# Performance work log

Measured on AMD Instinct MI355X. Metric: run time of the kernel, lower is better.

Reference implementation:

```python
import jax, jax.numpy as jnp
import numpy as np

N_NODES = 20000
N_EDGES = 160000
IN_DIM = 2048
HID = 512


def setup_inputs() -> dict:
    key = jax.random.key(0)
    ks = jax.random.split(key, 12)
    s1 = 1.0 / np.sqrt(IN_DIM)
    s2 = 1.0 / np.sqrt(HID)
    return {
        "x": jax.random.normal(ks[0], (N_NODES, IN_DIM), dtype=jnp.float32),
        "edge_index": jax.random.randint(ks[1], (2, N_EDGES), 0, N_NODES, dtype=jnp.int64),
        "W1": jax.random.uniform(ks[2], (IN_DIM, HID), jnp.float32, -s1, s1),
        "b1": jax.random.uniform(ks[3], (HID,), jnp.float32, -s1, s1),
        "W2": jax.random.uniform(ks[4], (HID, HID), jnp.float32, -s2, s2),
        "b2": jax.random.uniform(ks[5], (HID,), jnp.float32, -s2, s2),
        "Wg": jax.random.uniform(ks[6], (HID, HID), jnp.float32, -s2, s2),
        "bg": jax.random.uniform(ks[7], (HID,), jnp.float32, -s2, s2),
        "Wa": jax.random.uniform(ks[8], (HID, 1), jnp.float32, -s2, s2),
        "ba": jax.random.uniform(ks[9], (1,), jnp.float32, -s2, s2),
    }


def reference(x, edge_index, W1, b1, W2, b2, Wg, bg, Wa, ba):
    # GINConv (eps=0): h = MLP((1+eps)*x + sum_{j in N(i)} x_j)
    src, dst = edge_index[0], edge_index[1]
    agg = jax.ops.segment_sum(x[src], dst, num_segments=x.shape[0])  # [N, IN_DIM]
    h = x + agg
    h = jnp.maximum(h @ W1 + b1, 0.0) @ W2 + b2  # [N, HID]
    # Gated attention pooling scores
    A = jnp.tanh(h @ Wg + bg)                    # [N, HID]
    alpha = (A @ Wa + ba)[:, 0]                  # [N]
    att_scores = jax.nn.softmax(alpha, axis=0)   # softmax over all nodes
    return (h, att_scores)
```

## Files before the change

### kernel.cpp

```cpp
#include <hip/hip_runtime.h>

typedef __attribute__((ext_vector_type(8))) __bf16 bf16x8;
typedef __attribute__((ext_vector_type(4))) __bf16 bf16x4;
typedef __attribute__((ext_vector_type(4))) float f32x4;
typedef __attribute__((ext_vector_type(8))) unsigned short u16x8;

__device__ __forceinline__ bf16x8 cvt8(float4 a, float4 b) {
    bf16x8 o;
    o[0] = (__bf16)a.x; o[1] = (__bf16)a.y; o[2] = (__bf16)a.z; o[3] = (__bf16)a.w;
    o[4] = (__bf16)b.x; o[5] = (__bf16)b.y; o[6] = (__bf16)b.z; o[7] = (__bf16)b.w;
    return o;
}
__device__ __forceinline__ bf16x4 cvt4(f32x4 v) {
    bf16x4 o;
    o[0] = (__bf16)v[0]; o[1] = (__bf16)v[1]; o[2] = (__bf16)v[2]; o[3] = (__bf16)v[3];
    return o;
}

__device__ __forceinline__ unsigned swz(int row, int s) {
    return (unsigned)((row * 64 + s * 16) ^ ((row & 8) << 2));
}

__global__ __launch_bounds__(256) void convw_pre_kernel(const float* __restrict__ W,
                                                        char* __restrict__ out, int K) {
    int t = blockIdx.x * 256 + threadIdx.x;
    if (t >= K * 512) return;
    int k = t >> 9, n = t & 511;
    int cb = n >> 8, r = n & 255, tt = k >> 5, s = (k & 31) >> 3, e = k & 7;
    size_t off = ((size_t)cb * (K >> 5) + tt) * 16384 + swz(r, s) + e * 2;
    *(__bf16*)(out + off) = (__bf16)W[t];
}

__global__ __launch_bounds__(256) void count_kernel(const int* __restrict__ dst,
                                                    int* __restrict__ counts, int E) {
    int e = blockIdx.x * 256 + threadIdx.x;
    if (e < E) atomicAdd(&counts[dst[e]], 1);
}

__global__ __launch_bounds__(1024) void scan_kernel(const int* __restrict__ counts,
                                                    int* __restrict__ offs, int N) {
    __shared__ int wsum[16], wpre[16];
    const int CH = 20;
    int tid = threadIdx.x, lane = tid & 63, wv = tid >> 6;
    int base = tid * CH;
    int s = 0;
    for (int i = 0; i < CH; i++) { int idx = base + i; s += (idx < N) ? counts[idx] : 0; }
    int run = s;
#pragma unroll
    for (int o = 1; o < 64; o <<= 1) { int v = __shfl_up(run, o, 64); if (lane >= o) run += v; }
    if (lane == 63) wsum[wv] = run;
    __syncthreads();
    if (tid == 0) { int acc = 0; for (int w = 0; w < 16; w++) { wpre[w] = acc; acc += wsum[w]; } }
    __syncthreads();
    int pre = wpre[wv] + (run - s);
    for (int i = 0; i < CH; i++) {
        int idx = base + i;
        if (idx <= N) offs[idx] = pre;
        pre += (idx < N) ? counts[idx] : 0;
    }
}

__global__ __launch_bounds__(256) void bucket_kernel(const int* __restrict__ src,
                                                     const int* __restrict__ dst,
                                                     const int* __restrict__ offs,
                                                     int* __restrict__ cursor,
                                                     int* __restrict__ eids, int E) {
    int e = blockIdx.x * 256 + threadIdx.x;
    if (e >= E) return;
    int d = dst[e];
    int pos = atomicAdd(&cursor[d], 1);
    eids[offs[d] + pos] = src[e];
}

__global__ __launch_bounds__(256) void gather_h1_kernel(const float* __restrict__ y,
                                                        const int* __restrict__ offs,
                                                        const int* __restrict__ eids,
                                                        const float* __restrict__ b1,
                                                        __bf16* __restrict__ h1b,
                                                        int N) {
    int node = blockIdx.x * 2 + (threadIdx.x >> 7);
    if (node >= N) return;
    int c = (threadIdx.x & 127) << 2;
    float4 s = *(const float4*)(y + (size_t)node * 512 + c);
    int beg = offs[node], end = offs[node + 1];
    for (int k = beg; k < end; k++) {
        int sn = eids[k];
        const float4 v = *(const float4*)(y + (size_t)sn * 512 + c);
        s.x += v.x; s.y += v.y; s.z += v.z; s.w += v.w;
    }
    const float4 b = *(const float4*)(b1 + c);
    f32x4 r;
    r[0] = fmaxf(s.x + b.x, 0.f);
    r[1] = fmaxf(s.y + b.y, 0.f);
    r[2] = fmaxf(s.z + b.z, 0.f);
    r[3] = fmaxf(s.w + b.w, 0.f);
    *(bf16x4*)(h1b + (size_t)node * 512 + c) = cvt4(r);
}

template <int KDIM, int AMODE, int EPI>
__global__ __launch_bounds__(256) void gemm_nb(const void* __restrict__ Asrc,
                                               const char* __restrict__ Bpre,
                                               const float* __restrict__ bias,
                                               float* __restrict__ Cf,
                                               const float* __restrict__ Wa,
                                               float* __restrict__ alphaOut,
                                               int M) {
    constexpr int NT2 = KDIM / 64;
    __shared__ char smem[16384];
    const int tid = threadIdx.x, lane = tid & 63, wv = tid >> 6;
    const int fr = lane & 15, sec = lane >> 4, hi4 = (lane >> 4) * 4;
    const long row0 = (long)blockIdx.x * 64;
    const int cb = blockIdx.y;
    const char* Bp = Bpre + (size_t)cb * (KDIM / 32) * 16384;

    f32x4 acc[4][4];
#pragma unroll
    for (int m = 0; m < 4; m++)
#pragma unroll
        for (int n = 0; n < 4; n++)
#pragma unroll
            for (int r = 0; r < 4; r++) acc[m][n][r] = 0.f;

    const int ar_ = tid >> 2, ks = tid & 3;
    const unsigned awz = swz(ar_, ks);
    long arow = row0 + ar_; if (arow > (long)M - 1) arow = M - 1;
    const float* ApF = (const float*)Asrc + arow * KDIM;
    const char*  ApH = (const char*)Asrc + arow * (KDIM * 2);

#define ASEC(b) (smem + (b) * 8192)

    if constexpr (AMODE == 0) {
        float4 a0 = *(const float4*)(ApF + ks * 8);
        float4 a1 = *(const float4*)(ApF + ks * 8 + 4);
        float4 a2 = *(const float4*)(ApF + 32 + ks * 8);
        float4 a3 = *(const float4*)(ApF + 32 + ks * 8 + 4);
        *(bf16x8*)(ASEC(0) + awz) = cvt8(a0, a1);
        *(bf16x8*)(ASEC(0) + 4096 + awz) = cvt8(a2, a3);
    } else {
        u16x8 v0 = *(const u16x8*)(ApH + ks * 16);
        u16x8 v1 = *(const u16x8*)(ApH + 64 + ks * 16);
        *(u16x8*)(ASEC(0) + awz) = v0;
        *(u16x8*)(ASEC(0) + 4096 + awz) = v1;
    }
    asm volatile("s_waitcnt lgkmcnt(0)" ::: "memory");
    __builtin_amdgcn_s_barrier();

    int cur = 0;
    for (int tt = 0; tt < NT2; tt++) {
        const bool more = (tt + 1 < NT2);
        float4 a0, a1, a2, a3; u16x8 v0, v1;
        if (more) {
            if constexpr (AMODE == 0) {
                const float* p = ApF + (tt + 1) * 64;
                a0 = *(const float4*)(p + ks * 8);
                a1 = *(const float4*)(p + ks * 8 + 4);
                a2 = *(const float4*)(p + 32 + ks * 8);
                a3 = *(const float4*)(p + 32 + ks * 8 + 4);
            } else {
                const char* p = ApH + (size_t)(tt + 1) * 128;
                v0 = *(const u16x8*)(p + ks * 16);
                v1 = *(const u16x8*)(p + 64 + ks * 16);
            }
        }
#pragma unroll
        for (int h = 0; h < 2; h++) {
            const char* bt = Bp + (size_t)(tt * 2 + h) * 16384;
            bf16x8 wf[4], xf[4];
#pragma unroll
            for (int m = 0; m < 4; m++)
                wf[m] = *(const bf16x8*)(bt + swz(wv * 64 + m * 16 + fr, sec));
#pragma unroll
            for (int n = 0; n < 4; n++)
                xf[n] = *(const bf16x8*)(ASEC(cur) + h * 4096 + swz(n * 16 + fr, sec));
#pragma unroll
            for (int m = 0; m < 4; m++)
#pragma unroll
                for (int n = 0; n < 4; n++)
                    acc[m][n] = __builtin_amdgcn_mfma_f32_16x16x32_bf16(wf[m], xf[n], acc[m][n], 0, 0, 0);
        }
        if (more) {
            const int nxt = cur ^ 1;
            if constexpr (AMODE == 0) {
                *(bf16x8*)(ASEC(nxt) + awz) = cvt8(a0, a1);
                *(bf16x8*)(ASEC(nxt) + 4096 + awz) = cvt8(a2, a3);
            } else {
                *(u16x8*)(ASEC(nxt) + awz) = v0;
                *(u16x8*)(ASEC(nxt) + 4096 + awz) = v1;
            }
            asm volatile("s_waitcnt lgkmcnt(0)" ::: "memory");
            __builtin_amdgcn_s_barrier();
            cur = nxt;
        }
    }

    if constexpr (EPI == 0) {
#pragma unroll
        for (int n = 0; n < 4; n++) {
            long node = row0 + n * 16 + fr;
            if (node < M) {
#pragma unroll
                for (int m = 0; m < 4; m++)
                    *(f32x4*)(Cf + node * 512 + cb * 256 + wv * 64 + m * 16 + hi4) = acc[m][n];
            }
        }
    } else if constexpr (EPI == 1) {
#pragma unroll
        for (int n = 0; n < 4; n++) {
            long node = row0 + n * 16 + fr;
            if (node < M) {
#pragma unroll
                for (int m = 0; m < 4; m++) {
                    int hc = cb * 256 + wv * 64 + m * 16 + hi4;
                    f32x4 bv = *(const f32x4*)(bias + hc);
                    *(f32x4*)(Cf + node * 512 + hc) = acc[m][n] + bv;
                }
            }
        }
    } else {
        __syncthreads();
        float* aS = (float*)smem;
        if (tid < 64) aS[tid] = 0.f;
        __syncthreads();
#pragma unroll
        for (int n = 0; n < 4; n++) {
            float s = 0.f;
#pragma unroll
            for (int m = 0; m < 4; m++) {
                int gc = cb * 256 + wv * 64 + m * 16 + hi4;
                f32x4 bgv = *(const f32x4*)(bias + gc);
                f32x4 wav = *(const f32x4*)(Wa + gc);
#pragma unroll
                for (int r = 0; r < 4; r++)
                    s += tanhf(acc[m][n][r] + bgv[r]) * wav[r];
            }
            atomicAdd(&aS[n * 16 + fr], s);
        }
        __syncthreads();
        if (tid < 64) {
            long node = row0 + tid;
            if (node < M) atomicAdd(&alphaOut[node], aS[tid]);
        }
    }
#undef ASEC
}

__global__ __launch_bounds__(1024) void softmax_kernel(const float* __restrict__ alpha,
                                                       float* __restrict__ att, int N) {
    __shared__ float red[16];
    __shared__ float bc[2];
    int tid = threadIdx.x, lane = tid & 63, wv = tid >> 6;
    float m = -3.4e38f;
    for (int i = tid; i < N; i += 1024) m = fmaxf(m, alpha[i]);
#pragma unroll
    for (int o = 32; o > 0; o >>= 1) m = fmaxf(m, __shfl_xor(m, o, 64));
    if (lane == 0) red[wv] = m;
    __syncthreads();
    if (tid == 0) {
        float mm = red[0];
        for (int i = 1; i < 16; i++) mm = fmaxf(mm, red[i]);
        bc[0] = mm;
    }
    __syncthreads();
    float Mx = bc[0];
    float s = 0.f;
    for (int i = tid; i < N; i += 1024) s += expf(alpha[i] - Mx);
#pragma unroll
    for (int o = 32; o > 0; o >>= 1) s += __shfl_xor(s, o, 64);
    if (lane == 0) red[wv] = s;
    __syncthreads();
    if (tid == 0) {
        float ss = 0.f;
        for (int i = 0; i < 16; i++) ss += red[i];
        bc[1] = ss;
    }
    __syncthreads();
    float inv = 1.f / bc[1];
    for (int i = tid; i < N; i += 1024) att[i] = expf(alpha[i] - Mx) * inv;
}

extern "C" void kernel_launch(void* const* d_in, const int* in_sizes, int n_in,
                              void* d_out, int out_size, void* d_ws, size_t ws_size,
                              hipStream_t stream) {
    const float* x  = (const float*)d_in[0];
    const int*   ei = (const int*)d_in[1];
    const float* W1 = (const float*)d_in[2];
    const float* b1 = (const float*)d_in[3];
    const float* W2 = (const float*)d_in[4];
    const float* b2 = (const float*)d_in[5];
    const float* Wg = (const float*)d_in[6];
    const float* bg = (const float*)d_in[7];
    const float* Wa = (const float*)d_in[8];

    const int M = 20000, IN = 2048, H = 512, E = 160000;

    char* ws = (char*)d_ws;
    float* y      = (float*)ws;
    char*  W1p    = ws + 40960000;
    char*  W2p    = ws + 43057152;
    char*  Wgp    = ws + 43581440;
    __bf16* h1b   = (__bf16*)(ws + 44105728);
    float* alpha  = (float*)(ws + 64585728);
    int*   counts = (int*)(ws + 64665728);
    int*   offs   = (int*)(ws + 64745728);
    int*   cursor = (int*)(ws + 64825732);
    int*   eids   = (int*)(ws + 64905732);

    float* hout = (float*)d_out;
    float* att  = hout + (size_t)M * H;

    convw_pre_kernel<<<4096, 256, 0, stream>>>(W1, W1p, IN);
    convw_pre_kernel<<<1024, 256, 0, stream>>>(W2, W2p, H);
    convw_pre_kernel<<<1024, 256, 0, stream>>>(Wg, Wgp, H);

    hipMemsetAsync(counts, 0, M * 4, stream);
    count_kernel<<<(E + 255) / 256, 256, 0, stream>>>(ei + E, counts, E);
    scan_kernel<<<1, 1024, 0, stream>>>(counts, offs, M);
    hipMemsetAsync(cursor, 0, M * 4, stream);
    bucket_kernel<<<(E + 255) / 256, 256, 0, stream>>>(ei, ei + E, offs, cursor, eids, E);

    gemm_nb<2048, 0, 0><<<dim3(313, 2), 256, 0, stream>>>(x, W1p, nullptr, y, nullptr, nullptr, M);

    gather_h1_kernel<<<10000, 256, 0, stream>>>(y, offs, eids, b1, h1b, M);

    gemm_nb<512, 1, 1><<<dim3(313, 2), 256, 0, stream>>>(h1b, W2p, b2, hout, nullptr, nullptr, M);

    hipMemsetAsync(alpha, 0, M * 4, stream);
    gemm_nb<512, 0, 2><<<dim3(313, 2), 256, 0, stream>>>(hout, Wgp, bg, nullptr, Wa, alpha, M);

    softmax_kernel<<<1, 1024, 0, stream>>>(alpha, att, M);
}
```

Measured before the change: 279.9 us.

## Fuse W2 and gate GEMMs into one kernel; deepen GEMM1 prefetch pipeline

Replaces the separate W2 GEMM and gate/attention GEMM with one kernel. Each 512-thread block computes 32 full rows of h, stages them as bf16 in shared memory, and immediately runs the Wg GEMM plus the tanh/Wa reduction. This removes the re-read of h from global memory, one memset and a launch, and alpha is written directly without global atomics. The first GEMM is specialised and now prefetches A tiles two steps ahead and register-double-buffers the weight fragments, at the cost of more register pressure. The fused kernel assumes M is a multiple of 32 and has no bounds checks.

```diff
diff --git a/kernel.cpp b/kernel.cpp
--- a/kernel.cpp
+++ b/kernel.cpp
@@ -97,21 +97,15 @@
     *(bf16x4*)(h1b + (size_t)node * 512 + c) = cvt4(r);
 }
 
-template <int KDIM, int AMODE, int EPI>
-__global__ __launch_bounds__(256) void gemm_nb(const void* __restrict__ Asrc,
-                                               const char* __restrict__ Bpre,
-                                               const float* __restrict__ bias,
-                                               float* __restrict__ Cf,
-                                               const float* __restrict__ Wa,
-                                               float* __restrict__ alphaOut,
-                                               int M) {
-    constexpr int NT2 = KDIM / 64;
+__global__ __launch_bounds__(256) void gemm1_kernel(const float* __restrict__ X,
+                                                    const char* __restrict__ Bpre,
+                                                    float* __restrict__ Y, int M) {
+    constexpr int KDIM = 2048, NT2 = KDIM / 64;
     __shared__ char smem[16384];
     const int tid = threadIdx.x, lane = tid & 63, wv = tid >> 6;
     const int fr = lane & 15, sec = lane >> 4, hi4 = (lane >> 4) * 4;
     const long row0 = (long)blockIdx.x * 64;
-    const int cb = blockIdx.y;
-    const char* Bp = Bpre + (size_t)cb * (KDIM / 32) * 16384;
+    const char* Bp = Bpre + (size_t)blockIdx.y * 64 * 16384;
 
     f32x4 acc[4][4];
 #pragma unroll
@@ -124,51 +118,41 @@
     const int ar_ = tid >> 2, ks = tid & 3;
     const unsigned awz = swz(ar_, ks);
     long arow = row0 + ar_; if (arow > (long)M - 1) arow = M - 1;
-    const float* ApF = (const float*)Asrc + arow * KDIM;
-    const char*  ApH = (const char*)Asrc + arow * (KDIM * 2);
+    const float* Ap = X + arow * KDIM;
 
 #define ASEC(b) (smem + (b) * 8192)
-
-    if constexpr (AMODE == 0) {
-        float4 a0 = *(const float4*)(ApF + ks * 8);
-        float4 a1 = *(const float4*)(ApF + ks * 8 + 4);
-        float4 a2 = *(const float4*)(ApF + 32 + ks * 8);
-        float4 a3 = *(const float4*)(ApF + 32 + ks * 8 + 4);
-        *(bf16x8*)(ASEC(0) + awz) = cvt8(a0, a1);
-        *(bf16x8*)(ASEC(0) + 4096 + awz) = cvt8(a2, a3);
-    } else {
-        u16x8 v0 = *(const u16x8*)(ApH + ks * 16);
-        u16x8 v1 = *(const u16x8*)(ApH + 64 + ks * 16);
-        *(u16x8*)(ASEC(0) + awz) = v0;
-        *(u16x8*)(ASEC(0) + 4096 + awz) = v1;
-    }
+#define LOAD_A(d0, d1, d2, d3, t) do {                       \
+        const float* p_ = Ap + (t) * 64 + ks * 8;            \
+        d0 = *(const float4*)(p_);                           \
+        d1 = *(const float4*)(p_ + 4);                       \
+        d2 = *(const float4*)(p_ + 32);                      \
+        d3 = *(const float4*)(p_ + 36);                      \
+    } while (0)
+#define LOAD_WF(dst, g) do {                                              \
+        const char* bt_ = Bp + (size_t)(g) * 16384;                       \
+        _Pragma("unroll") for (int m_ = 0; m_ < 4; m_++)                  \
+            dst[m_] = *(const bf16x8*)(bt_ + swz(wv * 64 + m_ * 16 + fr, sec)); \
+    } while (0)
+
+    float4 aP0, aP1, aP2, aP3, aN0, aN1, aN2, aN3;
+    bf16x8 wfC[4], wfN[4];
+
+    LOAD_A(aP0, aP1, aP2, aP3, 0);
+    *(bf16x8*)(ASEC(0) + awz) = cvt8(aP0, aP1);
+    *(bf16x8*)(ASEC(0) + 4096 + awz) = cvt8(aP2, aP3);
+    LOAD_A(aP0, aP1, aP2, aP3, 1);
+    LOAD_A(aN0, aN1, aN2, aN3, 2);
+    LOAD_WF(wfC, 0);
     asm volatile("s_waitcnt lgkmcnt(0)" ::: "memory");
     __builtin_amdgcn_s_barrier();
 
     int cur = 0;
     for (int tt = 0; tt < NT2; tt++) {
-        const bool more = (tt + 1 < NT2);
-        float4 a0, a1, a2, a3; u16x8 v0, v1;
-        if (more) {
-            if constexpr (AMODE == 0) {
-                const float* p = ApF + (tt + 1) * 64;
-                a0 = *(const float4*)(p + ks * 8);
-                a1 = *(const float4*)(p + ks * 8 + 4);
-                a2 = *(const float4*)(p + 32 + ks * 8);
-                a3 = *(const float4*)(p + 32 + ks * 8 + 4);
-            } else {
-                const char* p = ApH + (size_t)(tt + 1) * 128;
-                v0 = *(const u16x8*)(p + ks * 16);
-                v1 = *(const u16x8*)(p + 64 + ks * 16);
-            }
-        }
 #pragma unroll
         for (int h = 0; h < 2; h++) {
-            const char* bt = Bp + (size_t)(tt * 2 + h) * 16384;
-            bf16x8 wf[4], xf[4];
-#pragma unroll
-            for (int m = 0; m < 4; m++)
-                wf[m] = *(const bf16x8*)(bt + swz(wv * 64 + m * 16 + fr, sec));
+            const int g = tt * 2 + h;
+            if (g + 1 < NT2 * 2) LOAD_WF(wfN, g + 1);
+            bf16x8 xf[4];
 #pragma unroll
             for (int n = 0; n < 4; n++)
                 xf[n] = *(const bf16x8*)(ASEC(cur) + h * 4096 + swz(n * 16 + fr, sec));
@@ -176,72 +160,174 @@
             for (int m = 0; m < 4; m++)
 #pragma unroll
                 for (int n = 0; n < 4; n++)
-                    acc[m][n] = __builtin_amdgcn_mfma_f32_16x16x32_bf16(wf[m], xf[n], acc[m][n], 0, 0, 0);
-        }
-        if (more) {
+                    acc[m][n] = __builtin_amdgcn_mfma_f32_16x16x32_bf16(wfC[m], xf[n], acc[m][n], 0, 0, 0);
+#pragma unroll
+            for (int m = 0; m < 4; m++) wfC[m] = wfN[m];
+        }
+        if (tt + 1 < NT2) {
             const int nxt = cur ^ 1;
-            if constexpr (AMODE == 0) {
-                *(bf16x8*)(ASEC(nxt) + awz) = cvt8(a0, a1);
-                *(bf16x8*)(ASEC(nxt) + 4096 + awz) = cvt8(a2, a3);
-            } else {
-                *(u16x8*)(ASEC(nxt) + awz) = v0;
-                *(u16x8*)(ASEC(nxt) + 4096 + awz) = v1;
-            }
+            *(bf16x8*)(ASEC(nxt) + awz) = cvt8(aP0, aP1);
+            *(bf16x8*)(ASEC(nxt) + 4096 + awz) = cvt8(aP2, aP3);
+            aP0 = aN0; aP1 = aN1; aP2 = aN2; aP3 = aN3;
+            if (tt + 3 < NT2) LOAD_A(aN0, aN1, aN2, aN3, tt + 3);
             asm volatile("s_waitcnt lgkmcnt(0)" ::: "memory");
             __builtin_amdgcn_s_barrier();
             cur = nxt;
         }
     }
-
-    if constexpr (EPI == 0) {
-#pragma unroll
-        for (int n = 0; n < 4; n++) {
-            long node = row0 + n * 16 + fr;
-            if (node < M) {
-#pragma unroll
-                for (int m = 0; m < 4; m++)
-                    *(f32x4*)(Cf + node * 512 + cb * 256 + wv * 64 + m * 16 + hi4) = acc[m][n];
-            }
-        }
-    } else if constexpr (EPI == 1) {
-#pragma unroll
-        for (int n = 0; n < 4; n++) {
-            long node = row0 + n * 16 + fr;
-            if (node < M) {
-#pragma unroll
-                for (int m = 0; m < 4; m++) {
-                    int hc = cb * 256 + wv * 64 + m * 16 + hi4;
-                    f32x4 bv = *(const f32x4*)(bias + hc);
-                    *(f32x4*)(Cf + node * 512 + hc) = acc[m][n] + bv;
-                }
-            }
-        }
-    } else {
-        __syncthreads();
-        float* aS = (float*)smem;
-        if (tid < 64) aS[tid] = 0.f;
-        __syncthreads();
-#pragma unroll
-        for (int n = 0; n < 4; n++) {
-            float s = 0.f;
-#pragma unroll
-            for (int m = 0; m < 4; m++) {
-                int gc = cb * 256 + wv * 64 + m * 16 + hi4;
-                f32x4 bgv = *(const f32x4*)(bias + gc);
-                f32x4 wav = *(const f32x4*)(Wa + gc);
-#pragma unroll
-                for (int r = 0; r < 4; r++)
-                    s += tanhf(acc[m][n][r] + bgv[r]) * wav[r];
-            }
-            atomicAdd(&aS[n * 16 + fr], s);
-        }
-        __syncthreads();
-        if (tid < 64) {
-            long node = row0 + tid;
-            if (node < M) atomicAdd(&alphaOut[node], aS[tid]);
-        }
-    }
 #undef ASEC
+#undef LOAD_A
+#undef LOAD_WF
+
+#pragma unroll
+    for (int n = 0; n < 4; n++) {
+        long node = row0 + n * 16 + fr;
+        if (node < M) {
+#pragma unroll
+            for (int m = 0; m < 4; m++)
+                *(f32x4*)(Y + node * 512 + blockIdx.y * 256 + wv * 64 + m * 16 + hi4) = acc[m][n];
+        }
+    }
+}
+
+__global__ __launch_bounds__(512) void mlp23_kernel(const __bf16* __restrict__ H1,
+                                                    const char* __restrict__ W2p,
+                                                    const float* __restrict__ b2,
+                                                    const char* __restrict__ Wgp,
+                                                    const float* __restrict__ bg,
+                                                    const float* __restrict__ Wa,
+                                                    float* __restrict__ Hout,
+                                                    float* __restrict__ alpha) {
+    constexpr int NT2 = 8;
+    __shared__ char smem[41216];
+    char* Hs = smem + 8192;
+    float* aS = (float*)(smem + 40960);
+    const int tid = threadIdx.x, lane = tid & 63, wv = tid >> 6;
+    const int fr = lane & 15, sec = lane >> 4, hi4 = (lane >> 4) * 4;
+    const long row0 = (long)blockIdx.x * 32;
+    const int cbv = wv >> 2, rbase = (wv & 3) * 64;
+
+    if (tid < 32) aS[tid] = 0.f;
+
+    const int srow = tid >> 3, sh = (tid & 7) >> 2, ss = tid & 3;
+    const unsigned awz = (unsigned)(sh * 2048) + swz(srow, ss);
+    const __bf16* ApH = H1 + (row0 + srow) * 512 + sh * 32 + ss * 8;
+
+#define ASEC(b) (smem + (b) * 4096)
+#define LOAD_WF(dst, img, g) do {                                         \
+        const char* bt_ = (img) + ((size_t)cbv * 16 + (g)) * 16384;       \
+        _Pragma("unroll") for (int m_ = 0; m_ < 4; m_++)                  \
+            dst[m_] = *(const bf16x8*)(bt_ + swz(rbase + m_ * 16 + fr, sec)); \
+    } while (0)
+
+    f32x4 acc[4][2];
+#pragma unroll
+    for (int m = 0; m < 4; m++)
+#pragma unroll
+        for (int n = 0; n < 2; n++)
+#pragma unroll
+            for (int r = 0; r < 4; r++) acc[m][n][r] = 0.f;
+
+    bf16x8 wfC[4], wfN[4];
+    if (tid < 256) {
+        u16x8 v = *(const u16x8*)(ApH);
+        *(u16x8*)(ASEC(0) + awz) = v;
+    }
+    LOAD_WF(wfC, W2p, 0);
+    asm volatile("s_waitcnt lgkmcnt(0)" ::: "memory");
+    __builtin_amdgcn_s_barrier();
+
+    int cur = 0;
+    for (int tt = 0; tt < NT2; tt++) {
+        u16x8 av;
+        const bool more = (tt + 1 < NT2);
+        if (more && tid < 256) av = *(const u16x8*)(ApH + (tt + 1) * 64);
+#pragma unroll
+        for (int h = 0; h < 2; h++) {
+            const int g = tt * 2 + h;
+            if (g + 1 < 16) LOAD_WF(wfN, W2p, g + 1);
+            bf16x8 xf[2];
+#pragma unroll
+            for (int n = 0; n < 2; n++)
+                xf[n] = *(const bf16x8*)(ASEC(cur) + h * 2048 + swz(n * 16 + fr, sec));
+#pragma unroll
+            for (int m = 0; m < 4; m++)
+#pragma unroll
+                for (int n = 0; n < 2; n++)
+                    acc[m][n] = __builtin_amdgcn_mfma_f32_16x16x32_bf16(wfC[m], xf[n], acc[m][n], 0, 0, 0);
+#pragma unroll
+            for (int m = 0; m < 4; m++) wfC[m] = wfN[m];
+        }
+        if (more) {
+            const int nxt = cur ^ 1;
+            if (tid < 256) *(u16x8*)(ASEC(nxt) + awz) = av;
+            asm volatile("s_waitcnt lgkmcnt(0)" ::: "memory");
+            __builtin_amdgcn_s_barrier();
+            cur = nxt;
+        }
+    }
+
+#pragma unroll
+    for (int n = 0; n < 2; n++) {
+        int node = n * 16 + fr;
+        long gnode = row0 + node;
+#pragma unroll
+        for (int m = 0; m < 4; m++) {
+            int hc = wv * 64 + m * 16 + hi4;
+            f32x4 bv = *(const f32x4*)(b2 + hc);
+            f32x4 v = acc[m][n] + bv;
+            *(f32x4*)(Hout + gnode * 512 + hc) = v;
+            int tt = hc >> 5, sk = (hc & 31) >> 3, e = hc & 7;
+            *(bf16x4*)(Hs + tt * 2048 + swz(node, sk) + e * 2) = cvt4(v);
+        }
+    }
+    asm volatile("s_waitcnt lgkmcnt(0)" ::: "memory");
+    __builtin_amdgcn_s_barrier();
+
+    f32x4 acc2[4][2];
+#pragma unroll
+    for (int m = 0; m < 4; m++)
+#pragma unroll
+        for (int n = 0; n < 2; n++)
+#pragma unroll
+            for (int r = 0; r < 4; r++) acc2[m][n][r] = 0.f;
+
+    LOAD_WF(wfC, Wgp, 0);
+    for (int g = 0; g < 16; g++) {
+        if (g + 1 < 16) LOAD_WF(wfN, Wgp, g + 1);
+        bf16x8 xf[2];
+#pragma unroll
+        for (int n = 0; n < 2; n++)
+            xf[n] = *(const bf16x8*)(Hs + g * 2048 + swz(n * 16 + fr, sec));
+#pragma unroll
+        for (int m = 0; m < 4; m++)
+#pragma unroll
+            for (int n = 0; n < 2; n++)
+                acc2[m][n] = __builtin_amdgcn_mfma_f32_16x16x32_bf16(wfC[m], xf[n], acc2[m][n], 0, 0, 0);
+#pragma unroll
+        for (int m = 0; m < 4; m++) wfC[m] = wfN[m];
+    }
+#undef ASEC
+#undef LOAD_WF
+
+#pragma unroll
+    for (int n = 0; n < 2; n++) {
+        float s = 0.f;
+#pragma unroll
+        for (int m = 0; m < 4; m++) {
+            int gc = wv * 64 + m * 16 + hi4;
+            f32x4 bgv = *(const f32x4*)(bg + gc);
+            f32x4 wav = *(const f32x4*)(Wa + gc);
+#pragma unroll
+            for (int r = 0; r < 4; r++)
+                s += tanhf(acc2[m][n][r] + bgv[r]) * wav[r];
+        }
+        s += __shfl_xor(s, 16, 64);
+        s += __shfl_xor(s, 32, 64);
+        if (sec == 0) atomicAdd(&aS[n * 16 + fr], s);
+    }
+    __syncthreads();
+    if (tid < 32) alpha[row0 + tid] = aS[tid];
 }
 
 __global__ __launch_bounds__(1024) void softmax_kernel(const float* __restrict__ alpha,
@@ -318,14 +404,11 @@
     hipMemsetAsync(cursor, 0, M * 4, stream);
     bucket_kernel<<<(E + 255) / 256, 256, 0, stream>>>(ei, ei + E, offs, cursor, eids, E);
 
-    gemm_nb<2048, 0, 0><<<dim3(313, 2), 256, 0, stream>>>(x, W1p, nullptr, y, nullptr, nullptr, M);
+    gemm1_kernel<<<dim3(313, 2), 256, 0, stream>>>(x, W1p, y, M);
 
     gather_h1_kernel<<<10000, 256, 0, stream>>>(y, offs, eids, b1, h1b, M);
 
-    gemm_nb<512, 1, 1><<<dim3(313, 2), 256, 0, stream>>>(h1b, W2p, b2, hout, nullptr, nullptr, M);
-
-    hipMemsetAsync(alpha, 0, M * 4, stream);
-    gemm_nb<512, 0, 2><<<dim3(313, 2), 256, 0, stream>>>(hout, Wgp, bg, nullptr, Wa, alpha, M);
+    mlp23_kernel<<<625, 512, 0, stream>>>(h1b, W2p, b2, Wgp, bg, Wa, hout, alpha);
 
     softmax_kernel<<<1, 1024, 0, stream>>>(alpha, att, M);
 }
```

After: 333.1 us. +19.0%, slower.
